# Performance work log

Measured on AMD Instinct MI355X. Metric: run time of the kernel, lower is better.

Reference implementation:

```python
import jax, jax.numpy as jnp
import numpy as np

IN_F, OUT_F, RANK = 4096, 4096, 64
B, S = 4, 2048


def setup_inputs() -> dict:
    key = jax.random.key(0)
    k1, k2, k3 = jax.random.split(key, 3)
    x = jax.random.normal(k1, (B, S, IN_F), dtype=jnp.float32)
    # Low-rank compressed weight factors: W = U @ V^T, shape [OUT_F, IN_F]
    U = jax.random.normal(k2, (OUT_F, RANK), dtype=jnp.float32) / np.sqrt(RANK)
    V = jax.random.normal(k3, (IN_F, RANK), dtype=jnp.float32) / np.sqrt(IN_F)
    bias = jnp.zeros((OUT_F,), dtype=jnp.float32)
    return {"x": x, "U": U, "V": V, "bias": bias}


def reference(x, U, V, bias):
    # Decompress: weight = compressor.decompress(compressed_weight) -> [out, in]
    weight = jnp.einsum("or,ir->oi", U, V)  # materialized like the original
    # F.linear(x, weight, bias) = x @ weight^T + bias
    return jnp.einsum("bsi,oi->bso", x, weight) + bias
```

## Files before the change

### kernel.cpp

```cpp
#include <hip/hip_runtime.h>

#define IN_F    4096
#define OUT_F   4096
#define RANK    64
#define M_TOTAL 8192
#define M_TILE  16
#define BLOCK   512
#define NWAVES  8

using short8  = __attribute__((ext_vector_type(8))) short;
using float4v = __attribute__((ext_vector_type(4))) float;

#define MFMA16(A, B, C) __builtin_amdgcn_mfma_f32_16x16x32_bf16((A), (B), (C), 0, 0, 0)

__device__ __forceinline__ void split2(float x, short& h, short& l) {
    unsigned u = __float_as_uint(x);
    unsigned t = u & 0xffff0000u;
    h = (short)(t >> 16);
    float r = x - __uint_as_float(t);
    l = (short)(__float_as_uint(r) >> 16);
}

__device__ __forceinline__ void split_f4x2(float4 a, float4 b, short8& hi, short8& lo) {
    short h0,h1,h2,h3,h4,h5,h6,h7, l0,l1,l2,l3,l4,l5,l6,l7;
    split2(a.x,h0,l0); split2(a.y,h1,l1); split2(a.z,h2,l2); split2(a.w,h3,l3);
    split2(b.x,h4,l4); split2(b.y,h5,l5); split2(b.z,h6,l6); split2(b.w,h7,l7);
    hi = (short8){h0,h1,h2,h3,h4,h5,h6,h7};
    lo = (short8){l0,l1,l2,l3,l4,l5,l6,l7};
}

__global__ void prep_v(const float* __restrict__ V, unsigned short* __restrict__ vt_hi,
                       unsigned short* __restrict__ vt_lo) {
    int linear = blockIdx.x * 256 + threadIdx.x;
    int r  = linear >> 10;
    int k0 = (linear & 1023) * 4;
    short h[4], l[4];
    #pragma unroll
    for (int i = 0; i < 4; ++i)
        split2(V[(size_t)(k0 + i) * RANK + r], h[i], l[i]);
    size_t o = (size_t)r * IN_F + k0;
    *(ushort4*)(vt_hi + o) = make_ushort4((unsigned short)h[0], (unsigned short)h[1],
                                          (unsigned short)h[2], (unsigned short)h[3]);
    *(ushort4*)(vt_lo + o) = make_ushort4((unsigned short)l[0], (unsigned short)l[1],
                                          (unsigned short)l[2], (unsigned short)l[3]);
}

__global__ __launch_bounds__(BLOCK, 4) void fused_lowrank_mfma(
    const float* __restrict__ x, const float* __restrict__ U,
    const float* __restrict__ bias, const unsigned short* __restrict__ vt_hi,
    const unsigned short* __restrict__ vt_lo, float* __restrict__ out)
{
    __shared__ float part[NWAVES][M_TILE][RANK + 4];
    __shared__ unsigned short t_hi[M_TILE][RANK + 8];
    __shared__ unsigned short t_lo[M_TILE][RANK + 8];

    const int tid  = threadIdx.x;
    const int wv   = tid >> 6;
    const int lane = tid & 63;
    const int l15  = lane & 15;
    const int quad = lane >> 4;
    const int m0   = blockIdx.x * M_TILE;

    float4v acc[4] = {};
    const float*          xp = x     + (size_t)(m0 + l15) * IN_F + quad * 8;
    const unsigned short* vh = vt_hi + (size_t)l15 * IN_F + quad * 8;
    const unsigned short* vl = vt_lo + (size_t)l15 * IN_F + quad * 8;

    #pragma unroll 2
    for (int ks = 0; ks < 16; ++ks) {
        const int k0 = wv * 512 + ks * 32;
        float4 xa = *(const float4*)(xp + k0);
        float4 xb = *(const float4*)(xp + k0 + 4);
        short8 a_hi, a_lo;
        split_f4x2(xa, xb, a_hi, a_lo);
        #pragma unroll
        for (int rt = 0; rt < 4; ++rt) {
            short8 b_hi = *(const short8*)(vh + (size_t)rt * 16 * IN_F + k0);
            short8 b_lo = *(const short8*)(vl + (size_t)rt * 16 * IN_F + k0);
            acc[rt] = MFMA16(a_lo, b_hi, acc[rt]);
            acc[rt] = MFMA16(a_hi, b_lo, acc[rt]);
            acc[rt] = MFMA16(a_hi, b_hi, acc[rt]);
        }
    }

    #pragma unroll
    for (int rt = 0; rt < 4; ++rt)
        #pragma unroll
        for (int rg = 0; rg < 4; ++rg)
            part[wv][quad * 4 + rg][rt * 16 + l15] = acc[rt][rg];
    __syncthreads();

    {
        const int e = tid * 2;
        const int m = e >> 6, r = e & 63;
        float s0 = 0.f, s1 = 0.f;
        #pragma unroll
        for (int w = 0; w < NWAVES; ++w) { s0 += part[w][m][r]; s1 += part[w][m][r + 1]; }
        short h0, l0, h1, l1;
        split2(s0, h0, l0); split2(s1, h1, l1);
        t_hi[m][r]     = (unsigned short)h0;  t_lo[m][r]     = (unsigned short)l0;
        t_hi[m][r + 1] = (unsigned short)h1;  t_lo[m][r + 1] = (unsigned short)l1;
    }
    __syncthreads();

    short8 ta_hi[2], ta_lo[2];
    #pragma unroll
    for (int ks = 0; ks < 2; ++ks) {
        ta_hi[ks] = *(const short8*)(&t_hi[l15][ks * 32 + quad * 8]);
        ta_lo[ks] = *(const short8*)(&t_lo[l15][ks * 32 + quad * 8]);
    }

    for (int nt = 0; nt < 32; ++nt) {
        const int o0 = wv * 512 + nt * 16;
        const int o  = o0 + l15;
        const float* Up = U + (size_t)o * RANK + quad * 8;
        const float bv = bias[o];
        float4v acc2 = {bv, bv, bv, bv};
        #pragma unroll
        for (int ks = 0; ks < 2; ++ks) {
            float4 u0 = *(const float4*)(Up + ks * 32);
            float4 u1 = *(const float4*)(Up + ks * 32 + 4);
            short8 u_hi, u_lo;
            split_f4x2(u0, u1, u_hi, u_lo);
            acc2 = MFMA16(ta_lo[ks], u_hi, acc2);
            acc2 = MFMA16(ta_hi[ks], u_lo, acc2);
            acc2 = MFMA16(ta_hi[ks], u_hi, acc2);
        }
        float* op = out + (size_t)(m0 + quad * 4) * OUT_F + o;
        op[0 * OUT_F] = acc2[0];
        op[1 * OUT_F] = acc2[1];
        op[2 * OUT_F] = acc2[2];
        op[3 * OUT_F] = acc2[3];
    }
}

__global__ __launch_bounds__(256, 2) void fallback_fp32(
    const float* __restrict__ x, const float* __restrict__ U,
    const float* __restrict__ V, const float* __restrict__ bias,
    float* __restrict__ out)
{
    __shared__ float v_lds[128][RANK];
    __shared__ float t_lds[8][RANK];
    const int tid = threadIdx.x, lane = tid & 63, wave = tid >> 6;
    const int m0 = blockIdx.x * 8;
    float acc0 = 0.f, acc1 = 0.f;
    const size_t row_base = (size_t)(m0 + wave * 2) * IN_F;
    for (int kt = 0; kt < IN_F; kt += 128) {
        const float4* Vg = (const float4*)(V + (size_t)kt * RANK);
        float4* Vs = (float4*)(&v_lds[0][0]);
        #pragma unroll
        for (int i = 0; i < 8; ++i) Vs[tid + 256 * i] = Vg[tid + 256 * i];
        __syncthreads();
        const float* xp = x + row_base + kt;
        #pragma unroll 8
        for (int k = 0; k < 128; k += 4) {
            float v0 = v_lds[k+0][lane], v1 = v_lds[k+1][lane];
            float v2 = v_lds[k+2][lane], v3 = v_lds[k+3][lane];
            float4 xa = *(const float4*)(xp + 0 * IN_F + k);
            float4 xb = *(const float4*)(xp + 1 * IN_F + k);
            acc0 += xa.x*v0 + xa.y*v1 + xa.z*v2 + xa.w*v3;
            acc1 += xb.x*v0 + xb.y*v1 + xb.z*v2 + xb.w*v3;
        }
        __syncthreads();
    }
    t_lds[wave*2+0][lane] = acc0;
    t_lds[wave*2+1][lane] = acc1;
    __syncthreads();
    for (int oc = 0; oc < OUT_F; oc += 1024) {
        const int o4 = oc + tid * 4;
        const float4 b4 = *(const float4*)(bias + o4);
        float4 a0=b4,a1=b4,a2=b4,a3=b4,a4=b4,a5=b4,a6=b4,a7=b4;
        const float* Up = U + (size_t)o4 * RANK;
        #pragma unroll 2
        for (int r0 = 0; r0 < RANK; r0 += 4) {
            const float4 u0 = *(const float4*)(Up + 0*RANK + r0);
            const float4 u1 = *(const float4*)(Up + 1*RANK + r0);
            const float4 u2 = *(const float4*)(Up + 2*RANK + r0);
            const float4 u3 = *(const float4*)(Up + 3*RANK + r0);
            #define P2_STEP(AM, MM) { \
                const float4 t4 = *(const float4*)(&t_lds[MM][r0]); \
                AM.x += t4.x*u0.x + t4.y*u0.y + t4.z*u0.z + t4.w*u0.w; \
                AM.y += t4.x*u1.x + t4.y*u1.y + t4.z*u1.z + t4.w*u1.w; \
                AM.z += t4.x*u2.x + t4.y*u2.y + t4.z*u2.z + t4.w*u2.w; \
                AM.w += t4.x*u3.x + t4.y*u3.y + t4.z*u3.z + t4.w*u3.w; }
            P2_STEP(a0,0) P2_STEP(a1,1) P2_STEP(a2,2) P2_STEP(a3,3)
            P2_STEP(a4,4) P2_STEP(a5,5) P2_STEP(a6,6) P2_STEP(a7,7)
            #undef P2_STEP
        }
        float* op = out + (size_t)m0 * OUT_F + o4;
        *(float4*)(op+0*OUT_F)=a0; *(float4*)(op+1*OUT_F)=a1;
        *(float4*)(op+2*OUT_F)=a2; *(float4*)(op+3*OUT_F)=a3;
        *(float4*)(op+4*OUT_F)=a4; *(float4*)(op+5*OUT_F)=a5;
        *(float4*)(op+6*OUT_F)=a6; *(float4*)(op+7*OUT_F)=a7;
    }
}

extern "C" void kernel_launch(void* const* d_in, const int* in_sizes, int n_in,
                              void* d_out, int out_size, void* d_ws, size_t ws_size,
                              hipStream_t stream) {
    const float* x    = (const float*)d_in[0];
    const float* U    = (const float*)d_in[1];
    const float* V    = (const float*)d_in[2];
    const float* bias = (const float*)d_in[3];
    float* out = (float*)d_out;

    const size_t need = (size_t)RANK * IN_F * sizeof(unsigned short) * 2;
    if (ws_size >= need) {
        unsigned short* vt_hi = (unsigned short*)d_ws;
        unsigned short* vt_lo = vt_hi + (size_t)RANK * IN_F;
        prep_v<<<dim3(256), dim3(256), 0, stream>>>(V, vt_hi, vt_lo);
        fused_lowrank_mfma<<<dim3(M_TOTAL / M_TILE), dim3(BLOCK), 0, stream>>>(
            x, U, bias, vt_hi, vt_lo, out);
    } else {
        fallback_fp32<<<dim3(M_TOTAL / 8), dim3(256), 0, stream>>>(x, U, V, bias, out);
    }
}
```

Measured before the change: 349.1 us.

## Split fused low-rank kernel into separate xV and tU kernels with pre-split U

Replaces the single fused kernel with three launches: a combined prep that pre-splits both V and U into bf16 hi/lo halves, a kernel computing T = xV that writes the split T to workspace, and a second kernel computing T·U^T + bias tiled over 64 rows × 512 outputs. The aim is to stop redoing the U fp32→bf16 split in every block and to spread the output-heavy second stage over a larger grid. It also adds a one-step register prefetch of x in the first stage. In exchange it costs an extra launch, a round trip of T through global memory, and a larger workspace requirement, with the old fused path kept as a fallback.

```diff
diff --git a/kernel.cpp b/kernel.cpp
--- a/kernel.cpp
+++ b/kernel.cpp
@@ -28,6 +28,145 @@
     hi = (short8){h0,h1,h2,h3,h4,h5,h6,h7};
     lo = (short8){l0,l1,l2,l3,l4,l5,l6,l7};
 }
+
+
+__global__ void prep_uv(const float* __restrict__ V, const float* __restrict__ U,
+                        unsigned short* __restrict__ vt_hi, unsigned short* __restrict__ vt_lo,
+                        unsigned short* __restrict__ u_hi,  unsigned short* __restrict__ u_lo)
+{
+    const int b = blockIdx.x;
+    const int linear = (b & 255) * 256 + threadIdx.x;
+    short h[4], l[4];
+    if (b < 256) {
+        const int r  = linear >> 10;
+        const int k0 = (linear & 1023) * 4;
+        #pragma unroll
+        for (int i = 0; i < 4; ++i)
+            split2(V[(size_t)(k0 + i) * RANK + r], h[i], l[i]);
+        const size_t o = (size_t)r * IN_F + k0;
+        *(ushort4*)(vt_hi + o) = make_ushort4((unsigned short)h[0], (unsigned short)h[1],
+                                              (unsigned short)h[2], (unsigned short)h[3]);
+        *(ushort4*)(vt_lo + o) = make_ushort4((unsigned short)l[0], (unsigned short)l[1],
+                                              (unsigned short)l[2], (unsigned short)l[3]);
+    } else {
+        const int idx = linear * 4;
+        const float4 u4 = *(const float4*)(U + idx);
+        split2(u4.x, h[0], l[0]); split2(u4.y, h[1], l[1]);
+        split2(u4.z, h[2], l[2]); split2(u4.w, h[3], l[3]);
+        *(ushort4*)(u_hi + idx) = make_ushort4((unsigned short)h[0], (unsigned short)h[1],
+                                               (unsigned short)h[2], (unsigned short)h[3]);
+        *(ushort4*)(u_lo + idx) = make_ushort4((unsigned short)l[0], (unsigned short)l[1],
+                                               (unsigned short)l[2], (unsigned short)l[3]);
+    }
+}
+
+__global__ __launch_bounds__(BLOCK, 4) void lowrank_xv(
+    const float* __restrict__ x,
+    const unsigned short* __restrict__ vt_hi, const unsigned short* __restrict__ vt_lo,
+    unsigned short* __restrict__ t_hi, unsigned short* __restrict__ t_lo)
+{
+    __shared__ float part[NWAVES][M_TILE][RANK + 4];
+
+    const int tid  = threadIdx.x;
+    const int wv   = tid >> 6;
+    const int lane = tid & 63;
+    const int l15  = lane & 15;
+    const int quad = lane >> 4;
+    const int m0   = blockIdx.x * M_TILE;
+
+    float4v acc[4] = {};
+    const float*          xp = x     + (size_t)(m0 + l15) * IN_F + wv * 512 + quad * 8;
+    const unsigned short* vh = vt_hi + (size_t)l15 * IN_F + wv * 512 + quad * 8;
+    const unsigned short* vl = vt_lo + (size_t)l15 * IN_F + wv * 512 + quad * 8;
+
+    float4 xa = *(const float4*)(xp);
+    float4 xb = *(const float4*)(xp + 4);
+    #pragma unroll
+    for (int ks = 0; ks < 16; ++ks) {
+        const int k0 = ks * 32;
+        float4 na = xa, nb = xb;
+        if (ks < 15) {
+            na = *(const float4*)(xp + k0 + 32);
+            nb = *(const float4*)(xp + k0 + 36);
+        }
+        short8 a_hi, a_lo;
+        split_f4x2(xa, xb, a_hi, a_lo);
+        #pragma unroll
+        for (int rt = 0; rt < 4; ++rt) {
+            short8 b_hi = *(const short8*)(vh + (size_t)rt * 16 * IN_F + k0);
+            short8 b_lo = *(const short8*)(vl + (size_t)rt * 16 * IN_F + k0);
+            acc[rt] = MFMA16(a_lo, b_hi, acc[rt]);
+            acc[rt] = MFMA16(a_hi, b_lo, acc[rt]);
+            acc[rt] = MFMA16(a_hi, b_hi, acc[rt]);
+        }
+        xa = na; xb = nb;
+    }
+
+    #pragma unroll
+    for (int rt = 0; rt < 4; ++rt)
+        #pragma unroll
+        for (int rg = 0; rg < 4; ++rg)
+            part[wv][quad * 4 + rg][rt * 16 + l15] = acc[rt][rg];
+    __syncthreads();
+
+    const int e = tid * 2;
+    const int m = e >> 6, r = e & 63;
+    float s0 = 0.f, s1 = 0.f;
+    #pragma unroll
+    for (int w = 0; w < NWAVES; ++w) { s0 += part[w][m][r]; s1 += part[w][m][r + 1]; }
+    short h0, l0, h1, l1;
+    split2(s0, h0, l0); split2(s1, h1, l1);
+    const size_t off = (size_t)m0 * RANK + e;
+    *(ushort2*)(t_hi + off) = make_ushort2((unsigned short)h0, (unsigned short)h1);
+    *(ushort2*)(t_lo + off) = make_ushort2((unsigned short)l0, (unsigned short)l1);
+}
+
+__global__ __launch_bounds__(256, 4) void lowrank_tu(
+    const unsigned short* __restrict__ t_hi, const unsigned short* __restrict__ t_lo,
+    const unsigned short* __restrict__ u_hi, const unsigned short* __restrict__ u_lo,
+    const float* __restrict__ bias, float* __restrict__ out)
+{
+    const int tid  = threadIdx.x;
+    const int wv   = tid >> 6;
+    const int lane = tid & 63;
+    const int l15  = lane & 15;
+    const int quad = lane >> 4;
+    const int og   = blockIdx.x & 7;
+    const int mg   = blockIdx.x >> 3;
+    const int m0   = mg * 64 + wv * 16;
+    const int o0   = og * 512;
+
+    short8 ta_hi[2], ta_lo[2];
+    {
+        const unsigned short* tp_h = t_hi + (size_t)(m0 + l15) * RANK + quad * 8;
+        const unsigned short* tp_l = t_lo + (size_t)(m0 + l15) * RANK + quad * 8;
+        ta_hi[0] = *(const short8*)(tp_h);   ta_hi[1] = *(const short8*)(tp_h + 32);
+        ta_lo[0] = *(const short8*)(tp_l);   ta_lo[1] = *(const short8*)(tp_l + 32);
+    }
+
+    #pragma unroll 2
+    for (int nt = 0; nt < 32; ++nt) {
+        const int o = o0 + nt * 16 + l15;
+        const unsigned short* up_h = u_hi + (size_t)o * RANK + quad * 8;
+        const unsigned short* up_l = u_lo + (size_t)o * RANK + quad * 8;
+        const float bv = bias[o];
+        float4v acc = {bv, bv, bv, bv};
+        #pragma unroll
+        for (int ks = 0; ks < 2; ++ks) {
+            short8 uh = *(const short8*)(up_h + ks * 32);
+            short8 ul = *(const short8*)(up_l + ks * 32);
+            acc = MFMA16(ta_lo[ks], uh, acc);
+            acc = MFMA16(ta_hi[ks], ul, acc);
+            acc = MFMA16(ta_hi[ks], uh, acc);
+        }
+        float* op = out + (size_t)(m0 + quad * 4) * OUT_F + o;
+        op[0 * OUT_F] = acc[0];
+        op[1 * OUT_F] = acc[1];
+        op[2 * OUT_F] = acc[2];
+        op[3 * OUT_F] = acc[3];
+    }
+}
+
 
 __global__ void prep_v(const float* __restrict__ V, unsigned short* __restrict__ vt_hi,
                        unsigned short* __restrict__ vt_lo) {
@@ -204,10 +343,26 @@
     const float* bias = (const float*)d_in[3];
     float* out = (float*)d_out;
 
-    const size_t need = (size_t)RANK * IN_F * sizeof(unsigned short) * 2;
-    if (ws_size >= need) {
+    const size_t E = (size_t)RANK * IN_F;
+    const size_t T = (size_t)M_TOTAL * RANK;
+    const size_t need_full  = (E * 4 + T * 2) * sizeof(unsigned short);
+    const size_t need_fused = (E * 2) * sizeof(unsigned short);
+
+    if (ws_size >= need_full) {
         unsigned short* vt_hi = (unsigned short*)d_ws;
-        unsigned short* vt_lo = vt_hi + (size_t)RANK * IN_F;
+        unsigned short* vt_lo = vt_hi + E;
+        unsigned short* u_hi  = vt_lo + E;
+        unsigned short* u_lo  = u_hi  + E;
+        unsigned short* t_hi  = u_lo  + E;
+        unsigned short* t_lo  = t_hi  + T;
+        prep_uv<<<dim3(512), dim3(256), 0, stream>>>(V, U, vt_hi, vt_lo, u_hi, u_lo);
+        lowrank_xv<<<dim3(M_TOTAL / M_TILE), dim3(BLOCK), 0, stream>>>(
+            x, vt_hi, vt_lo, t_hi, t_lo);
+        lowrank_tu<<<dim3((M_TOTAL / 64) * (OUT_F / 512)), dim3(256), 0, stream>>>(
+            t_hi, t_lo, u_hi, u_lo, bias, out);
+    } else if (ws_size >= need_fused) {
+        unsigned short* vt_hi = (unsigned short*)d_ws;
+        unsigned short* vt_lo = vt_hi + E;
         prep_v<<<dim3(256), dim3(256), 0, stream>>>(V, vt_hi, vt_lo);
         fused_lowrank_mfma<<<dim3(M_TOTAL / M_TILE), dim3(BLOCK), 0, stream>>>(
             x, U, bias, vt_hi, vt_lo, out);
```

Result: faster. 327.3 us (-6.2%).
